# Kernel optimization log

Hardware: AMD Instinct MI355X
Metric: run time of the kernel (lower is better)

The kernel has to match this reference:

```python
import jax, jax.numpy as jnp
import numpy as np

T, N, B, D = 64, 8, 128, 128      # time, n_agents, batch, obs_dim
H, S, K, A = 512, 64, 16, 16       # hidden_dim, subtask_dim, num_subtasks, action_dim
NB = N * B


def setup_inputs() -> dict:
    key = jax.random.key(0)
    ks = jax.random.split(key, 16)
    r = lambda i, shape: jax.random.normal(ks[i], shape, jnp.float32) * 0.02
    return dict(
        h1=jnp.zeros((NB, H), jnp.float32),
        h2=jnp.zeros((NB, H), jnp.float32),
        obs=jax.random.normal(ks[0], (T, N, B, D), jnp.float32),
        done=jax.random.bernoulli(ks[1], 0.05, (T, NB)),
        W_embed=r(2, (D, H)), b_embed=jnp.zeros((H,), jnp.float32),
        Wi1=r(3, (H, 3 * H)), bi1=jnp.zeros((3 * H,), jnp.float32),
        Wh1=r(4, (H, 3 * H)), bhn1=jnp.zeros((H,), jnp.float32),
        W_sub=r(5, (H, S)), b_sub=jnp.zeros((S,), jnp.float32),
        W_e1=r(6, (K, S)), b_e1=jnp.zeros((S,), jnp.float32),
        W_e2=r(7, (S, S)), b_e2=jnp.zeros((S,), jnp.float32),
        W_pol=r(8, (D, H)), b_pol=jnp.zeros((H,), jnp.float32),
        Wi2=r(9, (H, 3 * H)), bi2=jnp.zeros((3 * H,), jnp.float32),
        Wh2=r(10, (H, 3 * H)), bhn2=jnp.zeros((H,), jnp.float32),
        W_w1=r(11, (S, H * A)), b_w1=jnp.zeros((H * A,), jnp.float32),
        W_b1=r(12, (S, A)), b_b1=jnp.zeros((A,), jnp.float32),
    )


def _gru(h0, xs, dones, Wi, bi, Wh, bhn):
    """Flax GRUCell with per-step reset-to-zero carry (ScannedRNN)."""
    def step(h, inp):
        x, d = inp
        h = jnp.where(d[:, None], 0.0, h)          # reset carry on done
        gi = x @ Wi + bi                            # (NB, 3H): ir|iz|in
        gh = h @ Wh                                 # (NB, 3H): hr|hz|hn (hn bias separate)
        ir, iz, inn = jnp.split(gi, 3, axis=-1)
        hr, hz, hn = jnp.split(gh, 3, axis=-1)
        rg = jax.nn.sigmoid(ir + hr)
        zg = jax.nn.sigmoid(iz + hz)
        ng = jnp.tanh(inn + rg * (hn + bhn))
        hnew = (1.0 - zg) * ng + zg * h
        return hnew, hnew
    return jax.lax.scan(step, h0, (xs, dones))


def reference(h1, h2, obs, done, W_embed, b_embed, Wi1, bi1, Wh1, bhn1,
              W_sub, b_sub, W_e1, b_e1, W_e2, b_e2, W_pol, b_pol,
              Wi2, bi2, Wh2, bhn2, W_w1, b_w1, W_b1, b_b1):
    t, n, b, _ = obs.shape
    obs_f = obs.reshape(t, n * b, -1)                       # (T, NB, D)

    # agent embedding branch + GRU 1
    ae = jax.nn.relu(obs_f @ W_embed + b_embed)             # (T, NB, H)
    hT1, y1 = _gru(h1, ae, done, Wi1, bi1, Wh1, bhn1)
    ae2 = y1 @ W_sub + b_sub                                # (T, NB, S)
    ae2 = jnp.transpose(ae2.reshape(t, n, b, S), (0, 2, 1, 3))  # (T, B, N, S)

    # subtask embedding: input is eye(K), identical over (t, b) -> compute once
    e = jnp.tanh(jax.nn.relu(jnp.eye(K, dtype=obs.dtype) @ W_e1 + b_e1) @ W_e2 + b_e2)  # (K, S)
    subtask_embed = jnp.broadcast_to(e, (t, b, K, S))

    subtask_logits = jnp.einsum('tbns,ks->tbnk', ae2, e)    # (T, B, N, K)
    subtask_prob = jax.nn.one_hot(jnp.argmax(subtask_logits, axis=-1), K, dtype=obs.dtype)  # eval path

    # subtask policy branch + GRU 2
    sp = jax.nn.relu(obs_f @ W_pol + b_pol)                 # (T, NB, H)
    hT2, y2 = _gru(h2, sp, done, Wi2, bi2, Wh2, bhn2)

    # hypernetwork: _subtask_embed = stop_grad(subtask_embed[:, 0]) == e (time-invariant)
    e_sg = jax.lax.stop_gradient(e)
    w1 = (e_sg @ W_w1 + b_w1).reshape(K, H, A)              # (K, H, A)
    b1 = e_sg @ W_b1 + b_b1                                 # (K, A)

    # equivalent to the repeated-w1 batched matmul, without materializing (T,NB*K,H,A)
    q = jnp.einsum('tbh,kha->tbka', y2, w1) + b1            # (T, NB, K, A), NB in (N,B)-major order

    # faithful to original: prob flattened (B,N)-major vs q flattened (N,B)-major
    prob_flat = subtask_prob.reshape(t, b * n, K)
    q_vals = jnp.einsum('tbk,tbka->tba', prob_flat, q)      # (T, NB, A)

    return ((hT1, hT2), q_vals, subtask_logits, subtask_embed)
```

## Files before the change

### kernel.cpp

```cpp
#include <hip/hip_runtime.h>
#include <hip/hip_bf16.h>
#include <math.h>

#define TT 64
#define NN 8
#define BB 128
#define DD 128
#define HH 512
#define SS 64
#define KK 16
#define AA 16
#define NB 1024
#define H3 (3*HH)

typedef float f4v  __attribute__((ext_vector_type(4)));
typedef float f16v __attribute__((ext_vector_type(16)));
typedef short bf16x8 __attribute__((ext_vector_type(8)));

__device__ __forceinline__ float sigm(float x){ return 1.0f/(1.0f+expf(-x)); }
__device__ __forceinline__ unsigned short f2bf(float f){
  unsigned u = __float_as_uint(f);
  u += 0x7FFF + ((u >> 16) & 1);
  return (unsigned short)(u >> 16);
}
__device__ __forceinline__ float bf2f(unsigned short h){
  return __uint_as_float(((unsigned)h) << 16);
}

__global__ __launch_bounds__(256) void k_detect(const unsigned char* __restrict__ raw,
                                                int* __restrict__ flag)
{
  __shared__ int cA, cB;
  if (threadIdx.x == 0){ cA = 0; cB = 0; }
  __syncthreads();
  int a = 0, b = 0;
  for (int i = threadIdx.x; i < TT*NB; i += 256){
    unsigned char v = raw[i];
    if (v > 1) a++;
    if ((i & 3) != 0 && v != 0) b++;
  }
  atomicAdd(&cA, a); atomicAdd(&cB, b);
  __syncthreads();
  if (threadIdx.x == 0) *flag = (cB == 0) ? 0 : (cA == 0 ? 1 : 2);
}

__global__ __launch_bounds__(256) void k_mask(const unsigned char* __restrict__ raw,
                                              const int* __restrict__ flag,
                                              float* __restrict__ mask)
{
  int i = blockIdx.x*256 + threadIdx.x;
  if (i >= TT*NB) return;
  int f = *flag;
  int v;
  if (f == 1)      v = (int)raw[i];
  else if (f == 0) v = ((const int*)raw)[i];
  else             v = (((const float*)raw)[i] != 0.0f);
  mask[i] = v ? 0.f : 1.f;
}


__global__ __launch_bounds__(256) void k_e(const float* __restrict__ W_e1, const float* __restrict__ b_e1,
                                           const float* __restrict__ W_e2, const float* __restrict__ b_e2,
                                           float* __restrict__ e_out)
{
  __shared__ float r1[KK*SS];
  int tid = threadIdx.x;
  for (int i=0;i<4;++i){ int l = tid + i*256; float v = W_e1[l] + b_e1[l & 63]; r1[l] = v > 0.f ? v : 0.f; }
  __syncthreads();
  for (int i=0;i<4;++i){
    int l = tid + i*256; int k = l >> 6, s = l & 63;
    float acc = b_e2[s];
    #pragma unroll 8
    for (int sp=0; sp<64; ++sp) acc += r1[k*64+sp] * W_e2[sp*64 + s];
    e_out[l] = tanhf(acc);
  }
}

__global__ __launch_bounds__(256) void k_w1b1(const float* __restrict__ e, const float* __restrict__ W_w1,
                                              const float* __restrict__ b_w1, const float* __restrict__ W_b1,
                                              const float* __restrict__ b_b1, float* __restrict__ w1,
                                              float* __restrict__ b1)
{
  __shared__ float es[KK*SS];
  int tid = threadIdx.x;
  for (int i=0;i<4;++i) es[tid + i*256] = e[tid + i*256];
  __syncthreads();
  for (int i=0;i<4;++i){
    int l = blockIdx.x*1024 + tid + i*256;
    int k = l >> 13, m = l & 8191;
    float acc = b_w1[m];
    #pragma unroll 8
    for (int s=0;s<64;++s) acc += es[k*64+s] * W_w1[(size_t)s*8192 + m];
    w1[l] = acc;
  }
  if (blockIdx.x == 0){
    int k = tid >> 4, a = tid & 15;
    float acc = b_b1[a];
    #pragma unroll 8
    for (int s=0;s<64;++s) acc += es[k*64+s] * W_b1[s*16 + a];
    b1[tid] = acc;
  }
}

__global__ __launch_bounds__(256) void k_se(const float* __restrict__ e, float* __restrict__ outse)
{
  __shared__ float4 es[256];
  es[threadIdx.x] = ((const float4*)e)[threadIdx.x];
  __syncthreads();
  const int total4 = TT*BB*KK*SS/4;
  for (int i = blockIdx.x*256 + threadIdx.x; i < total4; i += gridDim.x*256)
    ((float4*)outse)[i] = es[i & 255];
}

__global__ void k_copy(const float* __restrict__ src, float* __restrict__ dst, int n4)
{
  int i = blockIdx.x*blockDim.x + threadIdx.x;
  if (i < n4) ((float4*)dst)[i] = ((const float4*)src)[i];
}

__global__ void k_merge(const unsigned short* __restrict__ h, const unsigned short* __restrict__ l,
                        float* __restrict__ o, int n8)
{
  int i = blockIdx.x*blockDim.x + threadIdx.x;
  if (i >= n8) return;
  uint4 vh = *(const uint4*)&h[(size_t)i*8];
  uint4 vl = *(const uint4*)&l[(size_t)i*8];
  const unsigned short* ph = (const unsigned short*)&vh;
  const unsigned short* pl = (const unsigned short*)&vl;
  float4 o0, o1;
  o0.x = bf2f(ph[0])+bf2f(pl[0]); o0.y = bf2f(ph[1])+bf2f(pl[1]);
  o0.z = bf2f(ph[2])+bf2f(pl[2]); o0.w = bf2f(ph[3])+bf2f(pl[3]);
  o1.x = bf2f(ph[4])+bf2f(pl[4]); o1.y = bf2f(ph[5])+bf2f(pl[5]);
  o1.z = bf2f(ph[6])+bf2f(pl[6]); o1.w = bf2f(ph[7])+bf2f(pl[7]);
  float4* d = (float4*)&o[(size_t)i*8];
  d[0] = o0; d[1] = o1;
}

__global__ void k_cast_bf16(const float* __restrict__ src, unsigned short* __restrict__ dst, int n8)
{
  int i = blockIdx.x*blockDim.x + threadIdx.x;
  if (i >= n8) return;
  const float4* s = (const float4*)(src + (size_t)i*8);
  float4 a = s[0], b = s[1];
  union { unsigned short u[8]; uint4 v; } p;
  p.u[0]=f2bf(a.x); p.u[1]=f2bf(a.y); p.u[2]=f2bf(a.z); p.u[3]=f2bf(a.w);
  p.u[4]=f2bf(b.x); p.u[5]=f2bf(b.y); p.u[6]=f2bf(b.z); p.u[7]=f2bf(b.w);
  *(uint4*)&dst[(size_t)i*8] = p.v;
}

__global__ __launch_bounds__(256) void k_tsplit(const float* __restrict__ W,
                                                unsigned short* __restrict__ WTh,
                                                unsigned short* __restrict__ WTl,
                                                int Kd, int Nc)
{
  __shared__ float t[32][33];
  int n0 = blockIdx.x * 32;
  int k0 = blockIdx.y * 32;
  int c = threadIdx.x & 31, r8 = threadIdx.x >> 5;
  for (int i=0;i<4;++i){
    int r = r8 + i*8;
    t[r][c] = W[(size_t)(k0+r)*Nc + n0 + c];
  }
  __syncthreads();
  for (int i=0;i<4;++i){
    int nr = r8 + i*8;
    float v = t[c][nr];
    unsigned short hi = f2bf(v);
    WTh[(size_t)(n0+nr)*Kd + k0 + c] = hi;
    WTl[(size_t)(n0+nr)*Kd + k0 + c] = f2bf(v - bf2f(hi));
  }
}

__global__ void k_split_cast(const float* __restrict__ src,
                             unsigned short* __restrict__ dh,
                             unsigned short* __restrict__ dl, int n8)
{
  int i = blockIdx.x*blockDim.x + threadIdx.x;
  if (i >= n8) return;
  const float4* s = (const float4*)(src + (size_t)i*8);
  float4 a = s[0], b = s[1];
  float x[8] = {a.x,a.y,a.z,a.w,b.x,b.y,b.z,b.w};
  union { unsigned short u[8]; uint4 v; } ph, pl;
  #pragma unroll
  for (int j=0;j<8;++j){
    unsigned short hi = f2bf(x[j]);
    ph.u[j] = hi;
    pl.u[j] = f2bf(x[j] - bf2f(hi));
  }
  *(uint4*)&dh[(size_t)i*8] = ph.v;
  *(uint4*)&dl[(size_t)i*8] = pl.v;
}

template<int KD, int SPLIT, int NTILE, int RELU, int OUTMODE>
__global__ __launch_bounds__(256) void mfma_gemm(
    const unsigned short* Ah, const unsigned short* Al,
    const unsigned short* Bh, const unsigned short* Bl,
    const float* __restrict__ bias,
    float* C, unsigned short* Chi, unsigned short* Clo, int Nstride)
{
  constexpr int NFC = NTILE/16;
  __shared__ __align__(16) unsigned short AsH[128*40];
  __shared__ __align__(16) unsigned short BsH[NTILE*40];
  __shared__ __align__(16) unsigned short AsL[SPLIT ? 128*40 : 8];
  __shared__ __align__(16) unsigned short BsL[SPLIT ? NTILE*40 : 8];
  int tid = threadIdx.x;
  int w = tid >> 6, l = tid & 63;
  int lr = l & 15, lk = (l >> 4) * 8, lq = l >> 4;
  int rowBase = blockIdx.y * 128, colBase = blockIdx.x * NTILE;
  f4v acc[2][NFC];
  f4v z = {0.f,0.f,0.f,0.f};
  #pragma unroll
  for (int i=0;i<2;++i)
    #pragma unroll
    for (int j=0;j<NFC;++j) acc[i][j] = z;

  for (int k0 = 0; k0 < KD; k0 += 32){
    {
      int r = tid >> 1, half = tid & 1;
      size_t src = (size_t)(rowBase + r)*KD + k0 + half*16;
      bf16x8* dA = (bf16x8*)&AsH[r*40 + half*16];
      dA[0] = *(const bf16x8*)&Ah[src];
      dA[1] = *(const bf16x8*)&Ah[src + 8];
      if (SPLIT){
        bf16x8* dL = (bf16x8*)&AsL[r*40 + half*16];
        dL[0] = *(const bf16x8*)&Al[src];
        dL[1] = *(const bf16x8*)&Al[src + 8];
      }
    }
    if (NTILE == 128){
      int r = tid >> 1, half = tid & 1;
      size_t src = (size_t)(colBase + r)*KD + k0 + half*16;
      bf16x8* dB = (bf16x8*)&BsH[r*40 + half*16];
      dB[0] = *(const bf16x8*)&Bh[src];
      dB[1] = *(const bf16x8*)&Bh[src + 8];
      if (SPLIT){
        bf16x8* dL = (bf16x8*)&BsL[r*40 + half*16];
        dL[0] = *(const bf16x8*)&Bl[src];
        dL[1] = *(const bf16x8*)&Bl[src + 8];
      }
    } else {
      int r = tid >> 2, q = tid & 3;
      size_t src = (size_t)(colBase + r)*KD + k0 + q*8;
      *(bf16x8*)&BsH[r*40 + q*8] = *(const bf16x8*)&Bh[src];
      if (SPLIT)
        *(bf16x8*)&BsL[r*40 + q*8] = *(const bf16x8*)&Bl[src];
    }
    __syncthreads();
    bf16x8 aH0 = *(const bf16x8*)&AsH[(w*32 + lr)*40 + lk];
    bf16x8 aH1 = *(const bf16x8*)&AsH[(w*32 + 16 + lr)*40 + lk];
    bf16x8 aL0, aL1;
    if (SPLIT){
      aL0 = *(const bf16x8*)&AsL[(w*32 + lr)*40 + lk];
      aL1 = *(const bf16x8*)&AsL[(w*32 + 16 + lr)*40 + lk];
    }
    #pragma unroll
    for (int fc=0; fc<NFC; ++fc){
      bf16x8 bH = *(const bf16x8*)&BsH[(fc*16 + lr)*40 + lk];
      acc[0][fc] = __builtin_amdgcn_mfma_f32_16x16x32_bf16(aH0, bH, acc[0][fc], 0,0,0);
      acc[1][fc] = __builtin_amdgcn_mfma_f32_16x16x32_bf16(aH1, bH, acc[1][fc], 0,0,0);
      if (SPLIT){
        bf16x8 bL = *(const bf16x8*)&BsL[(fc*16 + lr)*40 + lk];
        acc[0][fc] = __builtin_amdgcn_mfma_f32_16x16x32_bf16(aH0, bL, acc[0][fc], 0,0,0);
        acc[1][fc] = __builtin_amdgcn_mfma_f32_16x16x32_bf16(aH1, bL, acc[1][fc], 0,0,0);
        acc[0][fc] = __builtin_amdgcn_mfma_f32_16x16x32_bf16(aL0, bH, acc[0][fc], 0,0,0);
        acc[1][fc] = __builtin_amdgcn_mfma_f32_16x16x32_bf16(aL1, bH, acc[1][fc], 0,0,0);
      }
    }
    __syncthreads();
  }
  #pragma unroll
  for (int fr=0; fr<2; ++fr){
    #pragma unroll
    for (int fc=0; fc<NFC; ++fc){
      int col = colBase + fc*16 + lr;
      float bv = bias[col];
      #pragma unroll
      for (int r=0;r<4;++r){
        int row = rowBase + w*32 + fr*16 + lq*4 + r;
        float v = acc[fr][fc][r] + bv;
        if (RELU) v = v > 0.f ? v : 0.f;
        size_t o = (size_t)row*Nstride + col;
        if (OUTMODE == 0) C[o] = v;
        else if (OUTMODE == 1) Chi[o] = f2bf(v);
        else {
          unsigned short hi = f2bf(v);
          Chi[o] = hi;
          Clo[o] = f2bf(v - bf2f(hi));
        }
      }
    }
  }
}

__global__ __launch_bounds__(256) void gru_step_mix4(
    const unsigned short* __restrict__ hp1h, const unsigned short* __restrict__ hp1l,
    const float* __restrict__ hp2, const unsigned short* __restrict__ hp2b,
    const float* __restrict__ gi1, const float* __restrict__ gi2,
    const unsigned short* __restrict__ Wh1TH, const unsigned short* __restrict__ Wh1TL,
    const unsigned short* __restrict__ Wh2T,
    const float* __restrict__ bhn1, const float* __restrict__ bhn2,
    const float* __restrict__ mask_t,
    float* __restrict__ ho2, unsigned short* __restrict__ ho2b,
    unsigned short* __restrict__ y1h, unsigned short* __restrict__ y1l)
{
  __shared__ __align__(16) char smem[40960];
  int bid = blockIdx.x;
  int tid = threadIdx.x;
  int w = tid >> 6, l = tid & 63;
  int rf = w & 1, hc = w >> 1;
  int lc = l & 31, lh = l >> 5;
  int sr = tid >> 2, sg = tid & 3;
  f16v z16 = {0,0,0,0,0,0,0,0,0,0,0,0,0,0,0,0};
  uint4 zero4 = {0,0,0,0};

  if (bid < 128){
    unsigned short* As = (unsigned short*)smem;
    unsigned short* Bs = (unsigned short*)smem + 64*40;
    int ct = bid & 7, rt = bid >> 3;
    int rowBase = rt << 6, colBase = ct << 6;
    bool keep = mask_t[rowBase + sr] != 0.f;
    f16v acc[3] = {z16, z16, z16};

    uint4 pA;
    bf16x8 pB[3];
    {
      pA = *(const uint4*)&hp2b[(size_t)(rowBase + sr)*HH + sg*8];
      #pragma unroll
      for (int i=0;i<3;++i){
        int unit = i*256 + tid, brow = unit >> 2, q = unit & 3;
        int g = brow >> 6, c = brow & 63;
        pB[i] = *(const bf16x8*)&Wh2T[(size_t)(g*HH + colBase + c)*HH + q*8];
      }
    }
    for (int k0 = 0; k0 < HH; k0 += 32){
      __syncthreads();
      {
        *(uint4*)&As[sr*40 + sg*8] = keep ? pA : zero4;
        #pragma unroll
        for (int i=0;i<3;++i){
          int unit = i*256 + tid, brow = unit >> 2, q = unit & 3;
          *(bf16x8*)&Bs[brow*40 + q*8] = pB[i];
        }
      }
      __syncthreads();
      if (k0 + 32 < HH){
        pA = *(const uint4*)&hp2b[(size_t)(rowBase + sr)*HH + k0 + 32 + sg*8];
        #pragma unroll
        for (int i=0;i<3;++i){
          int unit = i*256 + tid, brow = unit >> 2, q = unit & 3;
          int g = brow >> 6, c = brow & 63;
          pB[i] = *(const bf16x8*)&Wh2T[(size_t)(g*HH + colBase + c)*HH + k0 + 32 + q*8];
        }
      }
      #pragma unroll
      for (int kc=0;kc<32;kc+=16){
        bf16x8 a = *(const bf16x8*)&As[(rf*32 + lc)*40 + kc + lh*8];
        #pragma unroll
        for (int g=0; g<3; ++g){
          bf16x8 b = *(const bf16x8*)&Bs[(g*64 + hc*32 + lc)*40 + kc + lh*8];
          acc[g] = __builtin_amdgcn_mfma_f32_32x32x16_bf16(a, b, acc[g], 0,0,0);
        }
      }
    }
    int col = colBase + hc*32 + lc;
    float bn = bhn2[col];
    #pragma unroll
    for (int r=0;r<16;++r){
      int row = rowBase + rf*32 + (r&3) + 8*(r>>2) + 4*lh;
      size_t gb = (size_t)row*H3 + col;
      float g_r = __builtin_nontemporal_load(&gi2[gb]);
      float g_z = __builtin_nontemporal_load(&gi2[gb + HH]);
      float g_n = __builtin_nontemporal_load(&gi2[gb + 2*HH]);
      float hv  = hp2[(size_t)row*HH + col] * mask_t[row];
      float rg = sigm(g_r + acc[0][r]);
      float zg = sigm(g_z + acc[1][r]);
      float ng = tanhf(g_n + rg*(acc[2][r] + bn));
      float o  = (1.f - zg)*ng + zg*hv;
      size_t oo = (size_t)row*HH + col;
      ho2[oo]  = o;
      ho2b[oo] = f2bf(o);
    }
  } else {
    unsigned short* AsH = (unsigned short*)smem;
    unsigned short* AsL = AsH + 64*40;
    unsigned short* BsH = AsL + 64*40;
    unsigned short* BsL = BsH + 192*40;
    int bidp = bid - 128;
    int ct = bidp & 7, rt = bidp >> 3;
    int rowBase = rt << 6, colBase = ct << 6;
    int capk = colBase + hc*32;
    bool keep = mask_t[rowBase + sr] != 0.f;
    f16v acc[3] = {z16, z16, z16};
    float hval[16];

    uint4 pAh, pAl;
    bf16x8 pBH[3], pBL[3];
    {
      size_t sA = (size_t)(rowBase + sr)*HH + sg*8;
      pAh = *(const uint4*)&hp1h[sA];
      pAl = *(const uint4*)&hp1l[sA];
      #pragma unroll
      for (int i=0;i<3;++i){
        int unit = i*256 + tid, brow = unit >> 2, q = unit & 3;
        int g = brow >> 6, c = brow & 63;
        size_t src = (size_t)(g*HH + colBase + c)*HH + q*8;
        pBH[i] = *(const bf16x8*)&Wh1TH[src];
        pBL[i] = *(const bf16x8*)&Wh1TL[src];
      }
    }
    for (int k0 = 0; k0 < HH; k0 += 32){
      __syncthreads();
      {
        *(uint4*)&AsH[sr*40 + sg*8] = keep ? pAh : zero4;
        *(uint4*)&AsL[sr*40 + sg*8] = keep ? pAl : zero4;
        #pragma unroll
        for (int i=0;i<3;++i){
          int unit = i*256 + tid, brow = unit >> 2, q = unit & 3;
          *(bf16x8*)&BsH[brow*40 + q*8] = pBH[i];
          *(bf16x8*)&BsL[brow*40 + q*8] = pBL[i];
        }
      }
      __syncthreads();
      if (k0 + 32 < HH){
        size_t sA = (size_t)(rowBase + sr)*HH + k0 + 32 + sg*8;
        pAh = *(const uint4*)&hp1h[sA];
        pAl = *(const uint4*)&hp1l[sA];
        #pragma unroll
        for (int i=0;i<3;++i){
          int unit = i*256 + tid, brow = unit >> 2, q = unit & 3;
          int g = brow >> 6, c = brow & 63;
          size_t src = (size_t)(g*HH + colBase + c)*HH + k0 + 32 + q*8;
          pBH[i] = *(const bf16x8*)&Wh1TH[src];
          pBL[i] = *(const bf16x8*)&Wh1TL[src];
        }
      }
      if (k0 == capk){
        #pragma unroll
        for (int r=0;r<16;++r){
          int rl = rf*32 + (r&3) + 8*(r>>2) + 4*lh;
          hval[r] = bf2f(AsH[rl*40 + lc]) + bf2f(AsL[rl*40 + lc]);
        }
      }
      #pragma unroll
      for (int kc=0;kc<32;kc+=16){
        bf16x8 aH = *(const bf16x8*)&AsH[(rf*32 + lc)*40 + kc + lh*8];
        bf16x8 aL = *(const bf16x8*)&AsL[(rf*32 + lc)*40 + kc + lh*8];
        #pragma unroll
        for (int g=0; g<3; ++g){
          int brow = (g*64 + hc*32 + lc)*40 + kc + lh*8;
          bf16x8 bH = *(const bf16x8*)&BsH[brow];
          bf16x8 bL = *(const bf16x8*)&BsL[brow];
          acc[g] = __builtin_amdgcn_mfma_f32_32x32x16_bf16(aH, bH, acc[g], 0,0,0);
          acc[g] = __builtin_amdgcn_mfma_f32_32x32x16_bf16(aH, bL, acc[g], 0,0,0);
          acc[g] = __builtin_amdgcn_mfma_f32_32x32x16_bf16(aL, bH, acc[g], 0,0,0);
        }
      }
    }
    int col = colBase + hc*32 + lc;
    float bn = bhn1[col];
    #pragma unroll
    for (int r=0;r<16;++r){
      int row = rowBase + rf*32 + (r&3) + 8*(r>>2) + 4*lh;
      size_t gb = (size_t)row*H3 + col;
      float g_r = __builtin_nontemporal_load(&gi1[gb]);
      float g_z = __builtin_nontemporal_load(&gi1[gb + HH]);
      float g_n = __builtin_nontemporal_load(&gi1[gb + 2*HH]);
      float rg = sigm(g_r + acc[0][r]);
      float zg = sigm(g_z + acc[1][r]);
      float ng = tanhf(g_n + rg*(acc[2][r] + bn));
      float o  = (1.f - zg)*ng + zg*hval[r];
      size_t oo = (size_t)row*HH + col;
      unsigned short hi = f2bf(o);
      y1h[oo] = hi;
      y1l[oo] = f2bf(o - bf2f(hi));
    }
  }
}

__global__ __launch_bounds__(256) void k_logits(const float* __restrict__ ae2,
    const float* __restrict__ e, float* __restrict__ out_logits, int* __restrict__ argk, int t0)
{
  __shared__ float es[KK*SS];
  int tid = threadIdx.x;
  for (int i=0;i<4;++i) es[tid + i*256] = e[tid + i*256];
  __syncthreads();
  int g = blockIdx.x*256 + tid;
  int t = t0 + (g >> 10), j = g & 1023;
  const float* arow = &ae2[(size_t)g * SS];
  float a[SS];
  #pragma unroll
  for (int i=0;i<16;++i){ float4 v = ((const float4*)arow)[i]; a[4*i]=v.x; a[4*i+1]=v.y; a[4*i+2]=v.z; a[4*i+3]=v.w; }
  float lg[KK];
  float best = -INFINITY; int bk = 0;
  #pragma unroll
  for (int k=0;k<KK;++k){
    float s2 = 0.f;
    #pragma unroll
    for (int s=0;s<SS;++s) s2 += a[s]*es[k*SS+s];
    lg[k] = s2;
    if (s2 > best){ best = s2; bk = k; }
  }
  int n = j >> 7, b = j & 127;
  size_t ob = ((size_t)((t*BB + b)*NN + n)) * KK;
  #pragma unroll
  for (int k4=0;k4<4;++k4)
    *(float4*)&out_logits[ob + k4*4] = make_float4(lg[k4*4],lg[k4*4+1],lg[k4*4+2],lg[k4*4+3]);
  argk[(t*BB + b)*NN + n] = bk;
}

__global__ __launch_bounds__(64) void k_qsel(const float* __restrict__ y2,
    const float* __restrict__ w1, const float* __restrict__ b1,
    const int* __restrict__ argk, float* __restrict__ outq)
{
  __shared__ float yr[HH];
  __shared__ float part[64];
  int bj = blockIdx.x;
  int tid = threadIdx.x;
  const float4* row4 = (const float4*)&y2[(size_t)bj*HH];
  ((float4*)yr)[tid]    = row4[tid];
  ((float4*)yr)[tid+64] = row4[tid+64];
  __syncthreads();
  int k = argk[bj];
  int a = tid & 15, q4 = tid >> 4;
  const float* wp = &w1[(size_t)k*HH*AA + a];
  float s = 0.f;
  int h0 = q4*128;
  #pragma unroll 8
  for (int h=h0; h<h0+128; ++h) s += yr[h]*wp[(size_t)h*AA];
  part[tid] = s;
  __syncthreads();
  if (q4 == 0){
    float v = part[a] + part[a+16] + part[a+32] + part[a+48] + b1[k*AA + a];
    outq[(size_t)bj*AA + a] = v;
  }
}

extern "C" void kernel_launch(void* const* d_in, const int* in_sizes, int n_in,
                              void* d_out, int out_size, void* d_ws, size_t ws_size,
                              hipStream_t stream)
{
  (void)in_sizes; (void)n_in; (void)out_size;
  const float* h1     = (const float*)d_in[0];
  const float* h2     = (const float*)d_in[1];
  const float* obs    = (const float*)d_in[2];
  const unsigned char* done_raw = (const unsigned char*)d_in[3];
  const float* W_embed=(const float*)d_in[4];  const float* b_embed=(const float*)d_in[5];
  const float* Wi1    =(const float*)d_in[6];  const float* bi1    =(const float*)d_in[7];
  const float* Wh1    =(const float*)d_in[8];  const float* bhn1   =(const float*)d_in[9];
  const float* W_sub  =(const float*)d_in[10]; const float* b_sub  =(const float*)d_in[11];
  const float* W_e1   =(const float*)d_in[12]; const float* b_e1   =(const float*)d_in[13];
  const float* W_e2   =(const float*)d_in[14]; const float* b_e2   =(const float*)d_in[15];
  const float* W_pol  =(const float*)d_in[16]; const float* b_pol  =(const float*)d_in[17];
  const float* Wi2    =(const float*)d_in[18]; const float* bi2    =(const float*)d_in[19];
  const float* Wh2    =(const float*)d_in[20]; const float* bhn2   =(const float*)d_in[21];
  const float* W_w1   =(const float*)d_in[22]; const float* b_w1   =(const float*)d_in[23];
  const float* W_b1   =(const float*)d_in[24]; const float* b_b1   =(const float*)d_in[25];

  float* out    = (float*)d_out;
  float* outHT1 = out;
  float* outHT2 = out + (size_t)NB*HH;
  float* outQ   = out + 2ull*NB*HH;
  float* outLG  = outQ + (size_t)TT*NB*AA;
  float* outSE  = outLG + (size_t)TT*BB*NN*KK;

  const size_t fixed_f = (size_t)TT*NB + 1024
                       + (size_t)KK*HH*AA + 256 + (size_t)TT*NB + 64
                       + 2ull*NB*HH/2
                       + 2ull*NB*HH/2
                       + 2ull*DD*HH/2 * 2
                       + 4ull*H3*HH
                       + (size_t)HH*SS;
  const size_t per_t_f = (size_t)NB*(HH + 2*H3 + SS)
                       + (size_t)NB*(HH/2 + DD + HH);
  int CH = 64;
  while (CH > 1 && (fixed_f + per_t_f*(size_t)CH)*4 > ws_size) CH >>= 1;

  float* buf2   = (float*)d_ws;
  float* gbuf1  = buf2   + (size_t)CH*NB*HH;
  float* gbuf2  = gbuf1  + (size_t)CH*NB*H3;
  float* ae2buf = gbuf2  + (size_t)CH*NB*H3;
  float* maskp  = ae2buf + (size_t)CH*NB*SS;
  float* ws_e   = maskp  + (size_t)TT*NB;
  float* ws_w1  = ws_e   + 1024;
  float* ws_b1  = ws_w1  + (size_t)KK*HH*AA;
  int*   ws_argk= (int*)(ws_b1 + 256);
  int*   ws_flag= (int*)(ws_argk + (size_t)TT*NB);
  unsigned short* buf2bf = (unsigned short*)(ws_flag + 64);
  unsigned short* obs_h  = buf2bf + (size_t)CH*NB*HH;
  unsigned short* obs_l  = obs_h  + (size_t)CH*NB*DD;
  unsigned short* y1_h   = obs_l  + (size_t)CH*NB*DD;
  unsigned short* y1_l   = y1_h   + (size_t)CH*NB*HH;
  unsigned short* hl1h   = y1_l   + (size_t)CH*NB*HH;
  unsigned short* hl1l   = hl1h   + (size_t)NB*HH;
  unsigned short* y2b0   = hl1l   + (size_t)NB*HH;
  unsigned short* y2b1   = y2b0   + (size_t)NB*HH;
  unsigned short* wembt_h= y2b1   + (size_t)NB*HH;
  unsigned short* wembt_l= wembt_h+ (size_t)HH*DD;
  unsigned short* wpolt_h= wembt_l+ (size_t)HH*DD;
  unsigned short* wpolt_l= wpolt_h+ (size_t)HH*DD;
  unsigned short* wi1t_h = wpolt_l+ (size_t)HH*DD;
  unsigned short* wi1t_l = wi1t_h + (size_t)H3*HH;
  unsigned short* wi2t_h = wi1t_l + (size_t)H3*HH;
  unsigned short* wi2t_l = wi2t_h + (size_t)H3*HH;
  unsigned short* wh1t_h = wi2t_l + (size_t)H3*HH;
  unsigned short* wh1t_l = wh1t_h + (size_t)H3*HH;
  unsigned short* wh2t_h = wh1t_l + (size_t)H3*HH;
  unsigned short* wh2t_l = wh2t_h + (size_t)H3*HH;
  unsigned short* wsubt_h= wh2t_l + (size_t)H3*HH;
  unsigned short* wsubt_l= wsubt_h+ (size_t)SS*HH;
  unsigned short* y2bslot[2] = { y2b0, y2b1 };

  k_detect<<<1,256,0,stream>>>(done_raw, ws_flag);
  k_mask<<<TT*NB/256,256,0,stream>>>(done_raw, ws_flag, maskp);
  k_e<<<1,256,0,stream>>>(W_e1,b_e1,W_e2,b_e2,ws_e);
  k_w1b1<<<128,256,0,stream>>>(ws_e,W_w1,b_w1,W_b1,b_b1,ws_w1,ws_b1);
  k_se<<<2048,256,0,stream>>>(ws_e,outSE);
  k_tsplit<<<dim3(16,4),256,0,stream>>>(W_embed, wembt_h, wembt_l, DD, HH);
  k_tsplit<<<dim3(16,4),256,0,stream>>>(W_pol,   wpolt_h, wpolt_l, DD, HH);
  k_tsplit<<<dim3(48,16),256,0,stream>>>(Wi1, wi1t_h, wi1t_l, HH, H3);
  k_tsplit<<<dim3(48,16),256,0,stream>>>(Wi2, wi2t_h, wi2t_l, HH, H3);
  k_tsplit<<<dim3(48,16),256,0,stream>>>(Wh1, wh1t_h, wh1t_l, HH, H3);
  k_tsplit<<<dim3(48,16),256,0,stream>>>(Wh2, wh2t_h, wh2t_l, HH, H3);
  k_tsplit<<<dim3(2,16),256,0,stream>>>(W_sub, wsubt_h, wsubt_l, HH, SS);
  k_split_cast<<<NB*HH/8/256,256,0,stream>>>(h1, hl1h, hl1l, NB*HH/8);
  k_cast_bf16<<<NB*HH/8/256,256,0,stream>>>(h2, y2b1, NB*HH/8);

  dim3 thr(256);
  const int NCH = TT / CH;
  for (int c = 0; c < NCH; ++c){
    int t0 = c * CH;
    int M = CH*NB;
    const float* obs_c = obs + (size_t)t0*NB*DD;
    k_split_cast<<<(M*DD/8+255)/256,256,0,stream>>>(obs_c, obs_h, obs_l, M*DD/8);
    mfma_gemm<DD,1,128,1,2><<<dim3(HH/128, M/128),thr,0,stream>>>(
        obs_h, obs_l, wembt_h, wembt_l, b_embed, nullptr, y1_h, y1_l, HH);
    mfma_gemm<HH,1,128,0,0><<<dim3(H3/128, M/128),thr,0,stream>>>(
        y1_h, y1_l, wi1t_h, wi1t_l, bi1, gbuf1, nullptr, nullptr, H3);
    mfma_gemm<DD,0,128,1,1><<<dim3(HH/128, M/128),thr,0,stream>>>(
        obs_h, obs_h, wpolt_h, wpolt_h, b_pol, nullptr, buf2bf, nullptr, HH);
    mfma_gemm<HH,0,128,0,0><<<dim3(H3/128, M/128),thr,0,stream>>>(
        buf2bf, buf2bf, wi2t_h, wi2t_h, bi2, gbuf2, nullptr, nullptr, H3);
    for (int lt = 0; lt < CH; ++lt){
      int gstep = t0 + lt;
      const unsigned short* hp1h = (lt == 0) ? hl1h : (y1_h + (size_t)(lt-1)*NB*HH);
      const unsigned short* hp1l = (lt == 0) ? hl1l : (y1_l + (size_t)(lt-1)*NB*HH);
      const float* hp2 = (c == 0 && lt == 0) ? h2 :
                         (lt == 0 ? buf2 + (size_t)(CH-1)*NB*HH : buf2 + (size_t)(lt-1)*NB*HH);
      const unsigned short* hp2b = y2bslot[(gstep+1)&1];
      gru_step_mix4<<<256, 256, 0, stream>>>(hp1h, hp1l, hp2, hp2b,
                                             gbuf1 + (size_t)lt*NB*H3, gbuf2 + (size_t)lt*NB*H3,
                                             wh1t_h, wh1t_l, wh2t_h, bhn1, bhn2,
                                             maskp + (size_t)gstep*NB,
                                             buf2 + (size_t)lt*NB*HH, y2bslot[gstep&1],
                                             y1_h + (size_t)lt*NB*HH, y1_l + (size_t)lt*NB*HH);
    }
    k_copy<<<256,256,0,stream>>>((const float*)(y1_h + (size_t)(CH-1)*NB*HH), (float*)hl1h, NB*HH/8);
    k_copy<<<256,256,0,stream>>>((const float*)(y1_l + (size_t)(CH-1)*NB*HH), (float*)hl1l, NB*HH/8);
    mfma_gemm<HH,1,64,0,0><<<dim3(1, M/128),thr,0,stream>>>(
        y1_h, y1_l, wsubt_h, wsubt_l, b_sub, ae2buf, nullptr, nullptr, SS);
    k_logits<<<M/256,256,0,stream>>>(ae2buf, ws_e, outLG, ws_argk, t0);
    k_qsel<<<M,64,0,stream>>>(buf2, ws_w1, ws_b1, ws_argk + (size_t)t0*NB, outQ + (size_t)t0*NB*AA);
  }
  k_merge<<<NB*HH/8/256,256,0,stream>>>(hl1h, hl1l, outHT1, NB*HH/8);
  k_copy<<<512,256,0,stream>>>(buf2 + (size_t)(CH-1)*NB*HH, outHT2, NB*HH/4);
}
```

Measured before the change: 3.303 ms.

## Double-buffer GRU step LDS tiles, interleave blocks, keep GRU2 hidden state only in bf16

The fused GRU step kernel now double-buffers its shared-memory tiles, using 80KB of dynamic LDS, so each k-chunk needs one barrier instead of two. Blocks alternate between GRU1 and GRU2 work by block-id parity. GRU2 no longer writes or reads an fp32 hidden state: the carry term comes from the bf16 A tile in LDS, and qsel and the final hT2 read the bf16 buffer. This cuts global traffic and synchronisation per step, but the GRU2 carry is now rounded to bf16 each step, which adds error, and the larger LDS footprint may lower occupancy.

Result: faster. 2.987 ms (-9.6%).

```diff
diff --git a/kernel.cpp b/kernel.cpp
--- a/kernel.cpp
+++ b/kernel.cpp
@@ -133,6 +133,18 @@
   o1.x = bf2f(ph[4])+bf2f(pl[4]); o1.y = bf2f(ph[5])+bf2f(pl[5]);
   o1.z = bf2f(ph[6])+bf2f(pl[6]); o1.w = bf2f(ph[7])+bf2f(pl[7]);
   float4* d = (float4*)&o[(size_t)i*8];
+  d[0] = o0; d[1] = o1;
+}
+
+__global__ void k_expand(const unsigned short* __restrict__ src, float* __restrict__ dst, int n8)
+{
+  int i = blockIdx.x*blockDim.x + threadIdx.x;
+  if (i >= n8) return;
+  uint4 v = *(const uint4*)&src[(size_t)i*8];
+  const unsigned short* p = (const unsigned short*)&v;
+  float4 o0 = make_float4(bf2f(p[0]),bf2f(p[1]),bf2f(p[2]),bf2f(p[3]));
+  float4 o1 = make_float4(bf2f(p[4]),bf2f(p[5]),bf2f(p[6]),bf2f(p[7]));
+  float4* d = (float4*)&dst[(size_t)i*8];
   d[0] = o0; d[1] = o1;
 }
 
@@ -292,75 +304,102 @@
   }
 }
 
-__global__ __launch_bounds__(256) void gru_step_mix4(
+__global__ __launch_bounds__(256) void gru_step_mix5(
     const unsigned short* __restrict__ hp1h, const unsigned short* __restrict__ hp1l,
-    const float* __restrict__ hp2, const unsigned short* __restrict__ hp2b,
+    const unsigned short* __restrict__ hp2b,
     const float* __restrict__ gi1, const float* __restrict__ gi2,
     const unsigned short* __restrict__ Wh1TH, const unsigned short* __restrict__ Wh1TL,
     const unsigned short* __restrict__ Wh2T,
     const float* __restrict__ bhn1, const float* __restrict__ bhn2,
     const float* __restrict__ mask_t,
-    float* __restrict__ ho2, unsigned short* __restrict__ ho2b,
+    unsigned short* __restrict__ y2b,
     unsigned short* __restrict__ y1h, unsigned short* __restrict__ y1l)
 {
-  __shared__ __align__(16) char smem[40960];
+  extern __shared__ __align__(16) char smem[];
   int bid = blockIdx.x;
   int tid = threadIdx.x;
   int w = tid >> 6, l = tid & 63;
   int rf = w & 1, hc = w >> 1;
   int lc = l & 31, lh = l >> 5;
   int sr = tid >> 2, sg = tid & 3;
+  int gru = bid & 1, sub = bid >> 1;
+  int ct = sub & 7, rt = sub >> 3;
+  int rowBase = rt << 6, colBase = ct << 6;
+  int capchunk = ct*2 + hc;
+  bool keep = mask_t[rowBase + sr] != 0.f;
   f16v z16 = {0,0,0,0,0,0,0,0,0,0,0,0,0,0,0,0};
   uint4 zero4 = {0,0,0,0};
 
-  if (bid < 128){
-    unsigned short* As = (unsigned short*)smem;
-    unsigned short* Bs = (unsigned short*)smem + 64*40;
-    int ct = bid & 7, rt = bid >> 3;
-    int rowBase = rt << 6, colBase = ct << 6;
-    bool keep = mask_t[rowBase + sr] != 0.f;
+  if (gru == 0){
     f16v acc[3] = {z16, z16, z16};
-
+    float hval[16];
     uint4 pA;
     bf16x8 pB[3];
+    pA = *(const uint4*)&hp2b[(size_t)(rowBase + sr)*HH + sg*8];
+    #pragma unroll
+    for (int i=0;i<3;++i){
+      int unit = i*256 + tid, brow = unit >> 2, q = unit & 3;
+      int g = brow >> 6, c = brow & 63;
+      pB[i] = *(const bf16x8*)&Wh2T[(size_t)(g*HH + colBase + c)*HH + q*8];
+    }
     {
-      pA = *(const uint4*)&hp2b[(size_t)(rowBase + sr)*HH + sg*8];
+      unsigned short* As0 = (unsigned short*)smem;
+      unsigned short* Bs0 = As0 + 64*40;
+      *(uint4*)&As0[sr*40 + sg*8] = keep ? pA : zero4;
       #pragma unroll
       for (int i=0;i<3;++i){
         int unit = i*256 + tid, brow = unit >> 2, q = unit & 3;
-        int g = brow >> 6, c = brow & 63;
-        pB[i] = *(const bf16x8*)&Wh2T[(size_t)(g*HH + colBase + c)*HH + q*8];
-      }
-    }
-    for (int k0 = 0; k0 < HH; k0 += 32){
-      __syncthreads();
-      {
-        *(uint4*)&As[sr*40 + sg*8] = keep ? pA : zero4;
+        *(bf16x8*)&Bs0[brow*40 + q*8] = pB[i];
+      }
+    }
+    pA = *(const uint4*)&hp2b[(size_t)(rowBase + sr)*HH + 32 + sg*8];
+    #pragma unroll
+    for (int i=0;i<3;++i){
+      int unit = i*256 + tid, brow = unit >> 2, q = unit & 3;
+      int g = brow >> 6, c = brow & 63;
+      pB[i] = *(const bf16x8*)&Wh2T[(size_t)(g*HH + colBase + c)*HH + 32 + q*8];
+    }
+    __syncthreads();
+    for (int ck = 0; ck < 16; ++ck){
+      unsigned short* Asc = (unsigned short*)(smem + (ck&1)*20480);
+      unsigned short* Bsc = Asc + 64*40;
+      if (ck < 15){
+        unsigned short* Asn = (unsigned short*)(smem + ((ck+1)&1)*20480);
+        unsigned short* Bsn = Asn + 64*40;
+        *(uint4*)&Asn[sr*40 + sg*8] = keep ? pA : zero4;
         #pragma unroll
         for (int i=0;i<3;++i){
           int unit = i*256 + tid, brow = unit >> 2, q = unit & 3;
-          *(bf16x8*)&Bs[brow*40 + q*8] = pB[i];
-        }
-      }
-      __syncthreads();
-      if (k0 + 32 < HH){
-        pA = *(const uint4*)&hp2b[(size_t)(rowBase + sr)*HH + k0 + 32 + sg*8];
+          *(bf16x8*)&Bsn[brow*40 + q*8] = pB[i];
+        }
+      }
+      if (ck < 14){
+        int k0 = (ck+2)*32;
+        pA = *(const uint4*)&hp2b[(size_t)(rowBase + sr)*HH + k0 + sg*8];
         #pragma unroll
         for (int i=0;i<3;++i){
           int unit = i*256 + tid, brow = unit >> 2, q = unit & 3;
           int g = brow >> 6, c = brow & 63;
-          pB[i] = *(const bf16x8*)&Wh2T[(size_t)(g*HH + colBase + c)*HH + k0 + 32 + q*8];
+          pB[i] = *(const bf16x8*)&Wh2T[(size_t)(g*HH + colBase + c)*HH + k0 + q*8];
+        }
+      }
+      if (ck == capchunk){
+        #pragma unroll
+        for (int r=0;r<16;++r){
+          int rl = rf*32 + (r&3) + 8*(r>>2) + 4*lh;
+          hval[r] = bf2f(Asc[rl*40 + lc]);
         }
       }
       #pragma unroll
       for (int kc=0;kc<32;kc+=16){
-        bf16x8 a = *(const bf16x8*)&As[(rf*32 + lc)*40 + kc + lh*8];
+        bf16x8 a = *(const bf16x8*)&Asc[(rf*32 + lc)*40 + kc + lh*8];
         #pragma unroll
         for (int g=0; g<3; ++g){
-          bf16x8 b = *(const bf16x8*)&Bs[(g*64 + hc*32 + lc)*40 + kc + lh*8];
+          bf16x8 b = *(const bf16x8*)&Bsc[(g*64 + hc*32 + lc)*40 + kc + lh*8];
           acc[g] = __builtin_amdgcn_mfma_f32_32x32x16_bf16(a, b, acc[g], 0,0,0);
         }
       }
+      __syncthreads();
     }
     int col = colBase + hc*32 + lc;
     float bn = bhn2[col];
@@ -371,90 +410,106 @@
       float g_r = __builtin_nontemporal_load(&gi2[gb]);
       float g_z = __builtin_nontemporal_load(&gi2[gb + HH]);
       float g_n = __builtin_nontemporal_load(&gi2[gb + 2*HH]);
-      float hv  = hp2[(size_t)row*HH + col] * mask_t[row];
       float rg = sigm(g_r + acc[0][r]);
       float zg = sigm(g_z + acc[1][r]);
       float ng = tanhf(g_n + rg*(acc[2][r] + bn));
-      float o  = (1.f - zg)*ng + zg*hv;
-      size_t oo = (size_t)row*HH + col;
-      ho2[oo]  = o;
-      ho2b[oo] = f2bf(o);
+      float o  = (1.f - zg)*ng + zg*hval[r];
+      y2b[(size_t)row*HH + col] = f2bf(o);
     }
   } else {
-    unsigned short* AsH = (unsigned short*)smem;
-    unsigned short* AsL = AsH + 64*40;
-    unsigned short* BsH = AsL + 64*40;
-    unsigned short* BsL = BsH + 192*40;
-    int bidp = bid - 128;
-    int ct = bidp & 7, rt = bidp >> 3;
-    int rowBase = rt << 6, colBase = ct << 6;
-    int capk = colBase + hc*32;
-    bool keep = mask_t[rowBase + sr] != 0.f;
     f16v acc[3] = {z16, z16, z16};
     float hval[16];
-
     uint4 pAh, pAl;
     bf16x8 pBH[3], pBL[3];
+    pAh = *(const uint4*)&hp1h[(size_t)(rowBase + sr)*HH + sg*8];
+    pAl = *(const uint4*)&hp1l[(size_t)(rowBase + sr)*HH + sg*8];
+    #pragma unroll
+    for (int i=0;i<3;++i){
+      int unit = i*256 + tid, brow = unit >> 2, q = unit & 3;
+      int g = brow >> 6, c = brow & 63;
+      size_t src = (size_t)(g*HH + colBase + c)*HH + q*8;
+      pBH[i] = *(const bf16x8*)&Wh1TH[src];
+      pBL[i] = *(const bf16x8*)&Wh1TL[src];
+    }
     {
-      size_t sA = (size_t)(rowBase + sr)*HH + sg*8;
-      pAh = *(const uint4*)&hp1h[sA];
-      pAl = *(const uint4*)&hp1l[sA];
+      unsigned short* AsH0 = (unsigned short*)smem;
+      unsigned short* AsL0 = AsH0 + 64*40;
+      unsigned short* BsH0 = AsL0 + 64*40;
+      unsigned short* BsL0 = BsH0 + 192*40;
+      *(uint4*)&AsH0[sr*40 + sg*8] = keep ? pAh : zero4;
+      *(uint4*)&AsL0[sr*40 + sg*8] = keep ? pAl : zero4;
       #pragma unroll
       for (int i=0;i<3;++i){
         int unit = i*256 + tid, brow = unit >> 2, q = unit & 3;
-        int g = brow >> 6, c = brow & 63;
-        size_t src = (size_t)(g*HH + colBase + c)*HH + q*8;
-        pBH[i] = *(const bf16x8*)&Wh1TH[src];
-        pBL[i] = *(const bf16x8*)&Wh1TL[src];
-      }
-    }
-    for (int k0 = 0; k0 < HH; k0 += 32){
-      __syncthreads();
-      {
-        *(uint4*)&AsH[sr*40 + sg*8] = keep ? pAh : zero4;
-        *(uint4*)&AsL[sr*40 + sg*8] = keep ? pAl : zero4;
+        *(bf16x8*)&BsH0[brow*40 + q*8] = pBH[i];
+        *(bf16x8*)&BsL0[brow*40 + q*8] = pBL[i];
+      }
+    }
+    pAh = *(const uint4*)&hp1h[(size_t)(rowBase + sr)*HH + 32 + sg*8];
+    pAl = *(const uint4*)&hp1l[(size_t)(rowBase + sr)*HH + 32 + sg*8];
+    #pragma unroll
+    for (int i=0;i<3;++i){
+      int unit = i*256 + tid, brow = unit >> 2, q = unit & 3;
+      int g = brow >> 6, c = brow & 63;
+      size_t src = (size_t)(g*HH + colBase + c)*HH + 32 + q*8;
+      pBH[i] = *(const bf16x8*)&Wh1TH[src];
+      pBL[i] = *(const bf16x8*)&Wh1TL[src];
+    }
+    __syncthreads();
+    for (int ck = 0; ck < 16; ++ck){
+      unsigned short* AsHc = (unsigned short*)(smem + (ck&1)*40960);
+      unsigned short* AsLc = AsHc + 64*40;
+      unsigned short* BsHc = AsLc + 64*40;
+      unsigned short* BsLc = BsHc + 192*40;
+      if (ck < 15){
+        unsigned short* AsHn = (unsigned short*)(smem + ((ck+1)&1)*40960);
+        unsigned short* AsLn = AsHn + 64*40;
+        unsigned short* BsHn = AsLn + 64*40;
+        unsigned short* BsLn = BsHn + 192*40;
+        *(uint4*)&AsHn[sr*40 + sg*8] = keep ? pAh : zero4;
+        *(uint4*)&AsLn[sr*40 + sg*8] = keep ? pAl : zero4;
         #pragma unroll
         for (int i=0;i<3;++i){
           int unit = i*256 + tid, brow = unit >> 2, q = unit & 3;
-          *(bf16x8*)&BsH[brow*40 + q*8] = pBH[i];
-          *(bf16x8*)&BsL[brow*40 + q*8] = pBL[i];
-        }
-      }
-      __syncthreads();
-      if (k0 + 32 < HH){
-        size_t sA = (size_t)(rowBase + sr)*HH + k0 + 32 + sg*8;
-        pAh = *(const uint4*)&hp1h[sA];
-        pAl = *(const uint4*)&hp1l[sA];
+          *(bf16x8*)&BsHn[brow*40 + q*8] = pBH[i];
+          *(bf16x8*)&BsLn[brow*40 + q*8] = pBL[i];
+        }
+      }
+      if (ck < 14){
+        int k0 = (ck+2)*32;
+        pAh = *(const uint4*)&hp1h[(size_t)(rowBase + sr)*HH + k0 + sg*8];
+        pAl = *(const uint4*)&hp1l[(size_t)(rowBase + sr)*HH + k0 + sg*8];
         #pragma unroll
         for (int i=0;i<3;++i){
           int unit = i*256 + tid, brow = unit >> 2, q = unit & 3;
           int g = brow >> 6, c = brow & 63;
-          size_t src = (size_t)(g*HH + colBase + c)*HH + k0 + 32 + q*8;
+          size_t src = (size_t)(g*HH + colBase + c)*HH + k0 + q*8;
           pBH[i] = *(const bf16x8*)&Wh1TH[src];
           pBL[i] = *(const bf16x8*)&Wh1TL[src];
         }
       }
-      if (k0 == capk){
+      if (ck == capchunk){
         #pragma unroll
         for (int r=0;r<16;++r){
           int rl = rf*32 + (r&3) + 8*(r>>2) + 4*lh;
-          hval[r] = bf2f(AsH[rl*40 + lc]) + bf2f(AsL[rl*40 + lc]);
+          hval[r] = bf2f(AsHc[rl*40 + lc]) + bf2f(AsLc[rl*40 + lc]);
         }
       }
       #pragma unroll
       for (int kc=0;kc<32;kc+=16){
-        bf16x8 aH = *(const bf16x8*)&AsH[(rf*32 + lc)*40 + kc + lh*8];
-        bf16x8 aL = *(const bf16x8*)&AsL[(rf*32 + lc)*40 + kc + lh*8];
+        bf16x8 aH = *(const bf16x8*)&AsHc[(rf*32 + lc)*40 + kc + lh*8];
+        bf16x8 aL = *(const bf16x8*)&AsLc[(rf*32 + lc)*40 + kc + lh*8];
         #pragma unroll
         for (int g=0; g<3; ++g){
           int brow = (g*64 + hc*32 + lc)*40 + kc + lh*8;
-          bf16x8 bH = *(const bf16x8*)&BsH[brow];
-          bf16x8 bL = *(const bf16x8*)&BsL[brow];
+          bf16x8 bH = *(const bf16x8*)&BsHc[brow];
+          bf16x8 bL = *(const bf16x8*)&BsLc[brow];
           acc[g] = __builtin_amdgcn_mfma_f32_32x32x16_bf16(aH, bH, acc[g], 0,0,0);
           acc[g] = __builtin_amdgcn_mfma_f32_32x32x16_bf16(aH, bL, acc[g], 0,0,0);
           acc[g] = __builtin_amdgcn_mfma_f32_32x32x16_bf16(aL, bH, acc[g], 0,0,0);
         }
       }
+      __syncthreads();
     }
     int col = colBase + hc*32 + lc;
     float bn = bhn1[col];
@@ -508,7 +563,7 @@
   argk[(t*BB + b)*NN + n] = bk;
 }
 
-__global__ __launch_bounds__(64) void k_qsel(const float* __restrict__ y2,
+__global__ __launch_bounds__(64) void k_qsel(const unsigned short* __restrict__ y2b,
     const float* __restrict__ w1, const float* __restrict__ b1,
     const int* __restrict__ argk, float* __restrict__ outq)
 {
@@ -516,9 +571,12 @@
   __shared__ float part[64];
   int bj = blockIdx.x;
   int tid = threadIdx.x;
-  const float4* row4 = (const float4*)&y2[(size_t)bj*HH];
-  ((float4*)yr)[tid]    = row4[tid];
-  ((float4*)yr)[tid+64] = row4[tid+64];
+  {
+    uint4 v = *(const uint4*)&y2b[(size_t)bj*HH + tid*8];
+    const unsigned short* p = (const unsigned short*)&v;
+    #pragma unroll
+    for (int j=0;j<8;++j) yr[tid*8 + j] = bf2f(p[j]);
+  }
   __syncthreads();
   int k = argk[bj];
   int a = tid & 15, q4 = tid >> 4;
@@ -566,17 +624,16 @@
   const size_t fixed_f = (size_t)TT*NB + 1024
                        + (size_t)KK*HH*AA + 256 + (size_t)TT*NB + 64
                        + 2ull*NB*HH/2
-                       + 2ull*NB*HH/2
+                       + (size_t)NB*HH/2
                        + 2ull*DD*HH/2 * 2
                        + 4ull*H3*HH
                        + (size_t)HH*SS;
-  const size_t per_t_f = (size_t)NB*(HH + 2*H3 + SS)
-                       + (size_t)NB*(HH/2 + DD + HH);
+  const size_t per_t_f = (size_t)NB*(2*H3 + SS)
+                       + (size_t)NB*(HH/2 + DD + HH + HH/2);
   int CH = 64;
   while (CH > 1 && (fixed_f + per_t_f*(size_t)CH)*4 > ws_size) CH >>= 1;
 
-  float* buf2   = (float*)d_ws;
-  float* gbuf1  = buf2   + (size_t)CH*NB*HH;
+  float* gbuf1  = (float*)d_ws;
   float* gbuf2  = gbuf1  + (size_t)CH*NB*H3;
   float* ae2buf = gbuf2  + (size_t)CH*NB*H3;
   float* maskp  = ae2buf + (size_t)CH*NB*SS;
@@ -590,11 +647,11 @@
   unsigned short* obs_l  = obs_h  + (size_t)CH*NB*DD;
   unsigned short* y1_h   = obs_l  + (size_t)CH*NB*DD;
   unsigned short* y1_l   = y1_h   + (size_t)CH*NB*HH;
-  unsigned short* hl1h   = y1_l   + (size_t)CH*NB*HH;
+  unsigned short* y2b    = y1_l   + (size_t)CH*NB*HH;
+  unsigned short* hl1h   = y2b    + (size_t)CH*NB*HH;
   unsigned short* hl1l   = hl1h   + (size_t)NB*HH;
-  unsigned short* y2b0   = hl1l   + (size_t)NB*HH;
-  unsigned short* y2b1   = y2b0   + (size_t)NB*HH;
-  unsigned short* wembt_h= y2b1   + (size_t)NB*HH;
+  unsigned short* h2b0   = hl1l   + (size_t)NB*HH;
+  unsigned short* wembt_h= h2b0   + (size_t)NB*HH;
   unsigned short* wembt_l= wembt_h+ (size_t)HH*DD;
   unsigned short* wpolt_h= wembt_l+ (size_t)HH*DD;
   unsigned short* wpolt_l= wpolt_h+ (size_t)HH*DD;
@@ -608,7 +665,9 @@
   unsigned short* wh2t_l = wh2t_h + (size_t)H3*HH;
   unsigned short* wsubt_h= wh2t_l + (size_t)H3*HH;
   unsigned short* wsubt_l= wsubt_h+ (size_t)SS*HH;
-  unsigned short* y2bslot[2] = { y2b0, y2b1 };
+
+  hipFuncSetAttribute((const void*)gru_step_mix5,
+                      hipFuncAttributeMaxDynamicSharedMemorySize, 81920);
 
   k_detect<<<1,256,0,stream>>>(done_raw, ws_flag);
   k_mask<<<TT*NB/256,256,0,stream>>>(done_raw, ws_flag, maskp);
@@ -623,7 +682,7 @@
   k_tsplit<<<dim3(48,16),256,0,stream>>>(Wh2, wh2t_h, wh2t_l, HH, H3);
   k_tsplit<<<dim3(2,16),256,0,stream>>>(W_sub, wsubt_h, wsubt_l, HH, SS);
   k_split_cast<<<NB*HH/8/256,256,0,stream>>>(h1, hl1h, hl1l, NB*HH/8);
-  k_cast_bf16<<<NB*HH/8/256,256,0,stream>>>(h2, y2b1, NB*HH/8);
+  k_cast_bf16<<<NB*HH/8/256,256,0,stream>>>(h2, h2b0, NB*HH/8);
 
   dim3 thr(256);
   const int NCH = TT / CH;
@@ -641,26 +700,25 @@
     mfma_gemm<HH,0,128,0,0><<<dim3(H3/128, M/128),thr,0,stream>>>(
         buf2bf, buf2bf, wi2t_h, wi2t_h, bi2, gbuf2, nullptr, nullptr, H3);
     for (int lt = 0; lt < CH; ++lt){
-      int gstep = t0 + lt;
       const unsigned short* hp1h = (lt == 0) ? hl1h : (y1_h + (size_t)(lt-1)*NB*HH);
       const unsigned short* hp1l = (lt == 0) ? hl1l : (y1_l + (size_t)(lt-1)*NB*HH);
-      const float* hp2 = (c == 0 && lt == 0) ? h2 :
-                         (lt == 0 ? buf2 + (size_t)(CH-1)*NB*HH : buf2 + (size_t)(lt-1)*NB*HH);
-      const unsigned short* hp2b = y2bslot[(gstep+1)&1];
-      gru_step_mix4<<<256, 256, 0, stream>>>(hp1h, hp1l, hp2, hp2b,
-                                             gbuf1 + (size_t)lt*NB*H3, gbuf2 + (size_t)lt*NB*H3,
-                                             wh1t_h, wh1t_l, wh2t_h, bhn1, bhn2,
-                                             maskp + (size_t)gstep*NB,
-                                             buf2 + (size_t)lt*NB*HH, y2bslot[gstep&1],
-                                             y1_h + (size_t)lt*NB*HH, y1_l + (size_t)lt*NB*HH);
+      const unsigned short* hp2b = (c == 0 && lt == 0) ? h2b0 :
+                                   (lt == 0 ? y2b + (size_t)(CH-1)*NB*HH
+                                            : y2b + (size_t)(lt-1)*NB*HH);
+      gru_step_mix5<<<256, 256, 81920, stream>>>(hp1h, hp1l, hp2b,
+                                                 gbuf1 + (size_t)lt*NB*H3, gbuf2 + (size_t)lt*NB*H3,
+                                                 wh1t_h, wh1t_l, wh2t_h, bhn1, bhn2,
+                                                 maskp + (size_t)(t0+lt)*NB,
+                                                 y2b + (size_t)lt*NB*HH,
+                                                 y1_h + (size_t)lt*NB*HH, y1_l + (size_t)lt*NB*HH);
     }
     k_copy<<<256,256,0,stream>>>((const float*)(y1_h + (size_t)(CH-1)*NB*HH), (float*)hl1h, NB*HH/8);
     k_copy<<<256,256,0,stream>>>((const float*)(y1_l + (size_t)(CH-1)*NB*HH), (float*)hl1l, NB*HH/8);
     mfma_gemm<HH,1,64,0,0><<<dim3(1, M/128),thr,0,stream>>>(
         y1_h, y1_l, wsubt_h, wsubt_l, b_sub, ae2buf, nullptr, nullptr, SS);
     k_logits<<<M/256,256,0,stream>>>(ae2buf, ws_e, outLG, ws_argk, t0);
-    k_qsel<<<M,64,0,stream>>>(buf2, ws_w1, ws_b1, ws_argk + (size_t)t0*NB, outQ + (size_t)t0*NB*AA);
+    k_qsel<<<M,64,0,stream>>>(y2b, ws_w1, ws_b1, ws_argk + (size_t)t0*NB, outQ + (size_t)t0*NB*AA);
   }
   k_merge<<<NB*HH/8/256,256,0,stream>>>(hl1h, hl1l, outHT1, NB*HH/8);
-  k_copy<<<512,256,0,stream>>>(buf2 + (size_t)(CH-1)*NB*HH, outHT2, NB*HH/4);
-}
+  k_expand<<<NB*HH/8/256,256,0,stream>>>(y2b + (size_t)(CH-1)*NB*HH, outHT2, NB*HH/8);
+}
```
